# Optimization experiments

Measured on AMD Instinct MI355X. Metric: run time of the kernel, lower is better.

The kernel has to match this reference:

```python
import jax, jax.numpy as jnp
import numpy as np

N, E, D, H, O = 100000, 1600000, 128, 64, 64


def setup_inputs() -> dict:
    key = jax.random.key(0)
    ks = jax.random.split(key, 6)
    src = jax.random.randint(ks[0], (E,), 0, N)
    dst = jax.random.randint(ks[1], (E,), 0, N)
    emb = jax.random.normal(ks[2], (N, D), jnp.float32) * 0.02  # embedding table
    W1 = jax.random.normal(ks[3], (D, H), jnp.float32) / np.sqrt(D)
    b1 = jnp.zeros((H,), jnp.float32)
    W2 = jax.random.normal(ks[4], (H, O), jnp.float32) / np.sqrt(H)
    b2 = jnp.zeros((O,), jnp.float32)
    return dict(emb=emb, W1=W1, b1=b1, W2=W2, b2=b2, src=src, dst=dst)


def gcn_conv(x, W, b, src, dst):
    # PyG GCNConv: add self-loops, symmetric deg^{-1/2} norm, linear -> gather -> scatter-add, bias
    n = x.shape[0]
    loop = jnp.arange(n, dtype=src.dtype)
    s = jnp.concatenate([src, loop])
    d = jnp.concatenate([dst, loop])
    x = x @ W  # [n, out]
    deg = jax.ops.segment_sum(jnp.ones_like(d, dtype=x.dtype), d, num_segments=n)
    dinv = jnp.where(deg > 0, jax.lax.rsqrt(deg), 0.0)
    norm = dinv[s] * dinv[d]  # [E+n]
    out = jax.ops.segment_sum(x[s] * norm[:, None], d, num_segments=n)
    return out + b


def reference(emb, W1, b1, W2, b2, src, dst):
    # node_ids = unique(edge_index) == arange(N) for contiguous ids -> lookup is whole table
    x = emb
    x = jax.nn.relu(gcn_conv(x, W1, b1, src, dst))
    return gcn_conv(x, W2, b2, src, dst)
```

## Files before the change

kernel.cpp:

```cpp
#include <hip/hip_runtime.h>

constexpr int FD = 64;
constexpr int P  = 8;
constexpr int WN = 125;
constexpr int SRC_BITS = 17;
constexpr int SRC_MASK = (1 << SRC_BITS) - 1;
constexpr int G1S = 16;

__device__ __forceinline__ int part_of(int d, unsigned long long M) {
    return (int)(((unsigned long long)(unsigned)d * M) >> 32);
}

__device__ __forceinline__ unsigned bf16pack(float a, float b) {
    unsigned ua = __float_as_uint(a), ub = __float_as_uint(b);
    ua = (ua + 0x7FFFu + ((ua >> 16) & 1u)) >> 16;
    ub = (ub + 0x7FFFu + ((ub >> 16) & 1u)) >> 16;
    return ua | (ub << 16);
}
__device__ __forceinline__ float4 bf16x4(uint2 u) {
    float4 v;
    v.x = __uint_as_float(u.x << 16);
    v.y = __uint_as_float(u.x & 0xFFFF0000u);
    v.z = __uint_as_float(u.y << 16);
    v.w = __uint_as_float(u.y & 0xFFFF0000u);
    return v;
}

__global__ void k_init(int* __restrict__ gcur1, int cap1,
                       int* __restrict__ gcur2, int cap2, int NW) {
    int i = threadIdx.x;
    if (i < P)  gcur1[i * G1S] = i * cap1;
    if (i < NW) gcur2[i] = i * cap2;
}

__global__ __launch_bounds__(256) void k_part8(const int* __restrict__ src,
                                               const int* __restrict__ dst, int E,
                                               unsigned long long M, int npp,
                                               int* __restrict__ gcur1, int cap1,
                                               int* __restrict__ p1) {
    constexpr int CH = 1024;
    __shared__ int hh[P], bbase[P], lcur[P];
    if (threadIdx.x < P) hh[threadIdx.x] = 0;
    __syncthreads();
    const int e0  = blockIdx.x * CH;
    const int rem = min(CH, E - e0);
    const int lane = threadIdx.x & 63;
    const unsigned long long lmlt = (lane == 63) ? ~0ull >> 1 : (1ull << lane) - 1;

    int dv[4], sv[4], bv[4], ldr[4], rnk[4], cnt[4];
    bool val[4];
    unsigned long long mm[4];
#pragma unroll
    for (int j = 0; j < 4; ++j) {
        int i = j * 256 + threadIdx.x;
        val[j] = i < rem;
        int e = e0 + (val[j] ? i : 0);
        dv[j] = __builtin_nontemporal_load(&dst[e]);
        sv[j] = __builtin_nontemporal_load(&src[e]);
        bv[j] = part_of(dv[j], M);
    }
#pragma unroll
    for (int j = 0; j < 4; ++j) {
        unsigned long long m0 = __ballot(val[j] && (bv[j] & 1));
        unsigned long long m1 = __ballot(val[j] && (bv[j] & 2));
        unsigned long long m2 = __ballot(val[j] && (bv[j] & 4));
        unsigned long long mv = __ballot(val[j]);
        unsigned long long t = ((bv[j] & 1) ? m0 : ~m0)
                             & ((bv[j] & 2) ? m1 : ~m1)
                             & ((bv[j] & 4) ? m2 : ~m2) & mv;
        mm[j]  = t;
        ldr[j] = __ffsll((unsigned long long)t) - 1;
        rnk[j] = __popcll(t & lmlt);
        cnt[j] = __popcll(t);
        if (val[j] && lane == ldr[j]) atomicAdd(&hh[bv[j]], cnt[j]);
    }
    __syncthreads();
    if (threadIdx.x < P) {
        bbase[threadIdx.x] = atomicAdd(&gcur1[threadIdx.x * G1S], hh[threadIdx.x]);
        lcur[threadIdx.x] = 0;
    }
    __syncthreads();
#pragma unroll
    for (int j = 0; j < 4; ++j) {
        int wb = 0;
        if (val[j] && lane == ldr[j]) wb = atomicAdd(&lcur[bv[j]], cnt[j]);
        wb = __shfl(wb, ldr[j] < 0 ? 0 : ldr[j], 64);
        if (val[j]) {
            int pos = bbase[bv[j]] + wb + rnk[j];
            if (pos < (bv[j] + 1) * cap1)
                p1[pos] = ((dv[j] - bv[j] * npp) << SRC_BITS) | sv[j];
        }
    }
}

__global__ __launch_bounds__(256) void k_partwin(const int* __restrict__ p1,
                                                 const int* __restrict__ gcur1, int cap1,
                                                 int npp, unsigned long long M2,
                                                 int* __restrict__ gcur2, int cap2,
                                                 int* __restrict__ p2) {
    constexpr int CH = 1024;
    constexpr int MAXW = 128;
    __shared__ int hh[MAXW], wbase[MAXW], lcur[MAXW];
    const int p   = blockIdx.x & (P - 1);
    const int j   = blockIdx.x >> 3;
    const int wlo = (p * npp) / WN;
    const int whi = ((p + 1) * npp - 1) / WN;
    const int nw  = whi - wlo + 1;
    const int lo = p * cap1 + j * CH;
    const int hi = min(lo + CH, gcur1[p * G1S]);
    if (lo >= hi) return;
    for (int t = threadIdx.x; t < nw; t += 256) hh[t] = 0;
    __syncthreads();
    int pk[4], wv[4];
    bool val[4];
#pragma unroll
    for (int q = 0; q < 4; ++q) {
        int e = lo + q * 256 + threadIdx.x;
        val[q] = e < hi;
        pk[q] = val[q] ? __builtin_nontemporal_load(&p1[e]) : 0;
        int d = p * npp + (pk[q] >> SRC_BITS);
        wv[q] = (int)(((unsigned long long)(unsigned)d * M2) >> 32);
        if (val[q]) atomicAdd(&hh[wv[q] - wlo], 1);
    }
    __syncthreads();
    for (int t = threadIdx.x; t < nw; t += 256) {
        wbase[t] = hh[t] ? atomicAdd(&gcur2[wlo + t], hh[t]) : 0;
        lcur[t] = 0;
    }
    __syncthreads();
#pragma unroll
    for (int q = 0; q < 4; ++q) {
        if (val[q]) {
            int w  = wv[q];
            int hw = w - wlo;
            int d  = p * npp + (pk[q] >> SRC_BITS);
            int pos = wbase[hw] + atomicAdd(&lcur[hw], 1);
            if (pos < (w + 1) * cap2)
                p2[pos] = ((d - w * WN) << SRC_BITS) | (pk[q] & SRC_MASK);
        }
    }
}

__global__ __launch_bounds__(256) void k_sortwin(int* __restrict__ p2,
                                                 const int* __restrict__ gcur2, int cap2,
                                                 int* __restrict__ rowinfo,
                                                 float* __restrict__ dinv, int N) {
    __shared__ int hist[WN], beg[WN], cur[WN];
    const int w  = blockIdx.x;
    const int lo = w * cap2;
    const int hi = min(gcur2[w], lo + cap2);
    const int cnt = hi - lo;
    for (int t = threadIdx.x; t < WN; t += 256) hist[t] = 0;
    __syncthreads();
    int pk[10];
#pragma unroll
    for (int j = 0; j < 10; ++j) {
        int i = j * 256 + threadIdx.x;
        pk[j] = (i < cnt) ? p2[lo + i] : -1;
        if (pk[j] >= 0) atomicAdd(&hist[pk[j] >> SRC_BITS], 1);
    }
    __syncthreads();
    if (threadIdx.x < 64) {
        int lane = threadIdx.x;
        int v0 = hist[lane];
        int x0 = v0;
#pragma unroll
        for (int o = 1; o < 64; o <<= 1) { int y = __shfl_up(x0, o, 64); if (lane >= o) x0 += y; }
        int tot0 = __shfl(x0, 63, 64);
        int v1 = (lane < WN - 64) ? hist[64 + lane] : 0;
        int x1 = v1;
#pragma unroll
        for (int o = 1; o < 64; o <<= 1) { int y = __shfl_up(x1, o, 64); if (lane >= o) x1 += y; }
        int b0 = x0 - v0;
        beg[lane] = b0; cur[lane] = b0;
        if (lane < WN - 64) {
            int b1 = tot0 + x1 - v1;
            beg[64 + lane] = b1; cur[64 + lane] = b1;
        }
    }
    __syncthreads();
#pragma unroll
    for (int j = 0; j < 10; ++j) {
        if (pk[j] >= 0) {
            int ld  = pk[j] >> SRC_BITS;
            int pos = atomicAdd(&cur[ld], 1);
            p2[lo + pos] = pk[j] & SRC_MASK;
        }
    }
    for (int t = threadIdx.x; t < WN; t += 256) {
        int node = w * WN + t;
        if (node < N) {
            rowinfo[node] = beg[t] | (hist[t] << 16);
            dinv[node] = rsqrtf((float)(hist[t] + 1));
        }
    }
}

template <int K, bool RELU>
__global__ __launch_bounds__(256) void k_gemm(const float* __restrict__ X,
                                              const float* __restrict__ W,
                                              const float* __restrict__ dinv,
                                              unsigned* __restrict__ Yb, int n) {
    constexpr int ASTR = 260;
    __shared__ __align__(16) float Bs[K * FD];
    __shared__ __align__(16) float As[32 * ASTR];
    for (int i = threadIdx.x; i < K * FD / 4; i += 256)
        ((float4*)Bs)[i] = ((const float4*)W)[i];

    const int rt   = threadIdx.x >> 3;
    const int ct   = threadIdx.x & 7;
    const int row0 = blockIdx.x * 256;
    float acc[8][8] = {};

    for (int kp = 0; kp < K; kp += 32) {
        __syncthreads();
        const int mq = threadIdx.x >> 3;
        const int q  = threadIdx.x & 7;
        float4 tv[8];
#pragma unroll
        for (int pass = 0; pass < 8; ++pass) {
            int grow = row0 + mq + pass * 32;
            float4 v = make_float4(0.f, 0.f, 0.f, 0.f);
            if (grow < n) {
                v = *(const float4*)&X[(size_t)grow * K + kp + q * 4];
                if (RELU) {
                    v.x = fmaxf(v.x, 0.f); v.y = fmaxf(v.y, 0.f);
                    v.z = fmaxf(v.z, 0.f); v.w = fmaxf(v.w, 0.f);
                }
            }
            tv[pass] = v;
        }
#pragma unroll
        for (int pass = 0; pass < 8; ++pass) {
            int m = mq + pass * 32;
            As[(q * 4 + 0) * ASTR + m] = tv[pass].x;
            As[(q * 4 + 1) * ASTR + m] = tv[pass].y;
            As[(q * 4 + 2) * ASTR + m] = tv[pass].z;
            As[(q * 4 + 3) * ASTR + m] = tv[pass].w;
        }
        __syncthreads();
#pragma unroll 8
        for (int k = 0; k < 32; ++k) {
            float4 a0 = *(const float4*)&As[k * ASTR + rt * 8];
            float4 a1 = *(const float4*)&As[k * ASTR + rt * 8 + 4];
            float4 b0 = *(const float4*)&Bs[(kp + k) * FD + ct * 8];
            float4 b1 = *(const float4*)&Bs[(kp + k) * FD + ct * 8 + 4];
            float af[8] = {a0.x, a0.y, a0.z, a0.w, a1.x, a1.y, a1.z, a1.w};
            float bf[8] = {b0.x, b0.y, b0.z, b0.w, b1.x, b1.y, b1.z, b1.w};
#pragma unroll
            for (int i = 0; i < 8; ++i)
#pragma unroll
                for (int j = 0; j < 8; ++j)
                    acc[i][j] = fmaf(af[i], bf[j], acc[i][j]);
        }
    }
#pragma unroll
    for (int i = 0; i < 8; ++i) {
        int r = row0 + rt * 8 + i;
        if (r < n) {
            float sc = dinv[r];
            uint4 w;
            w.x = bf16pack(acc[i][0] * sc, acc[i][1] * sc);
            w.y = bf16pack(acc[i][2] * sc, acc[i][3] * sc);
            w.z = bf16pack(acc[i][4] * sc, acc[i][5] * sc);
            w.w = bf16pack(acc[i][6] * sc, acc[i][7] * sc);
            ((uint4*)Yb)[(size_t)r * 8 + ct] = w;
        }
    }
}

__global__ __launch_bounds__(256) void k_agg(const unsigned* __restrict__ Xb,
                                             const int* __restrict__ col,
                                             const int* __restrict__ rowinfo, int cap2,
                                             const float* __restrict__ dinv,
                                             const float* __restrict__ bias,
                                             float* __restrict__ out, int n) {
    int t = blockIdx.x * 256 + threadIdx.x;
    int node = t >> 4;
    int lane = t & 15;
    if (node >= n) return;
    int info = rowinfo[node];
    int w    = (int)((unsigned)node / WN);
    int beg  = w * cap2 + (info & 0xFFFF);
    int end  = beg + (info >> 16);
    const uint2* Xv = (const uint2*)Xb;
    uint2 svu = Xv[(size_t)node * 16 + lane];
    float4 a0 = {0,0,0,0}, a1 = {0,0,0,0}, a2 = {0,0,0,0}, a3 = {0,0,0,0};
    int e = beg;
    for (; e + 8 <= end; e += 8) {
        int s0 = col[e],     s1 = col[e + 1], s2 = col[e + 2], s3 = col[e + 3];
        int s4 = col[e + 4], s5 = col[e + 5], s6 = col[e + 6], s7 = col[e + 7];
        uint2 u0 = Xv[(size_t)s0 * 16 + lane];
        uint2 u1 = Xv[(size_t)s1 * 16 + lane];
        uint2 u2 = Xv[(size_t)s2 * 16 + lane];
        uint2 u3 = Xv[(size_t)s3 * 16 + lane];
        uint2 u4 = Xv[(size_t)s4 * 16 + lane];
        uint2 u5 = Xv[(size_t)s5 * 16 + lane];
        uint2 u6 = Xv[(size_t)s6 * 16 + lane];
        uint2 u7 = Xv[(size_t)s7 * 16 + lane];
        float4 v0 = bf16x4(u0), v1 = bf16x4(u1), v2 = bf16x4(u2), v3 = bf16x4(u3);
        float4 v4 = bf16x4(u4), v5 = bf16x4(u5), v6 = bf16x4(u6), v7 = bf16x4(u7);
        a0.x += v0.x; a0.y += v0.y; a0.z += v0.z; a0.w += v0.w;
        a1.x += v1.x; a1.y += v1.y; a1.z += v1.z; a1.w += v1.w;
        a2.x += v2.x; a2.y += v2.y; a2.z += v2.z; a2.w += v2.w;
        a3.x += v3.x; a3.y += v3.y; a3.z += v3.z; a3.w += v3.w;
        a0.x += v4.x; a0.y += v4.y; a0.z += v4.z; a0.w += v4.w;
        a1.x += v5.x; a1.y += v5.y; a1.z += v5.z; a1.w += v5.w;
        a2.x += v6.x; a2.y += v6.y; a2.z += v6.z; a2.w += v6.w;
        a3.x += v7.x; a3.y += v7.y; a3.z += v7.z; a3.w += v7.w;
    }
    for (; e + 4 <= end; e += 4) {
        int s0 = col[e], s1 = col[e + 1], s2 = col[e + 2], s3 = col[e + 3];
        uint2 u0 = Xv[(size_t)s0 * 16 + lane];
        uint2 u1 = Xv[(size_t)s1 * 16 + lane];
        uint2 u2 = Xv[(size_t)s2 * 16 + lane];
        uint2 u3 = Xv[(size_t)s3 * 16 + lane];
        float4 v0 = bf16x4(u0), v1 = bf16x4(u1), v2 = bf16x4(u2), v3 = bf16x4(u3);
        a0.x += v0.x; a0.y += v0.y; a0.z += v0.z; a0.w += v0.w;
        a1.x += v1.x; a1.y += v1.y; a1.z += v1.z; a1.w += v1.w;
        a2.x += v2.x; a2.y += v2.y; a2.z += v2.z; a2.w += v2.w;
        a3.x += v3.x; a3.y += v3.y; a3.z += v3.z; a3.w += v3.w;
    }
    for (; e < end; ++e) {
        float4 v = bf16x4(Xv[(size_t)col[e] * 16 + lane]);
        a0.x += v.x; a0.y += v.y; a0.z += v.z; a0.w += v.w;
    }
    float4 sv = bf16x4(svu);
    float sx = a0.x + a1.x + a2.x + a3.x + sv.x;
    float sy = a0.y + a1.y + a2.y + a3.y + sv.y;
    float sz = a0.z + a1.z + a2.z + a3.z + sv.z;
    float sw = a0.w + a1.w + a2.w + a3.w + sv.w;
    float di = dinv[node];
    float4 b = ((const float4*)bias)[lane];
    float4 o;
    o.x = fmaf(di, sx, b.x);
    o.y = fmaf(di, sy, b.y);
    o.z = fmaf(di, sz, b.z);
    o.w = fmaf(di, sw, b.w);
    ((float4*)(out + (size_t)node * FD))[lane] = o;
}


extern "C" void kernel_launch(void* const* d_in, const int* in_sizes, int n_in,
                              void* d_out, int out_size, void* d_ws, size_t ws_size,
                              hipStream_t stream) {
    const float* emb = (const float*)d_in[0];
    const float* W1  = (const float*)d_in[1];
    const float* b1  = (const float*)d_in[2];
    const float* W2  = (const float*)d_in[3];
    const float* b2  = (const float*)d_in[4];
    const int*   src = (const int*)d_in[5];
    const int*   dst = (const int*)d_in[6];

    const int D = 128;
    const int N = in_sizes[0] / D;
    const int E = in_sizes[5];
    float* out = (float*)d_out;

    const int npp  = (N + P - 1) / P;
    const int NW   = (N + WN - 1) / WN;
    const int cap1 = E / P + 16384;
    int cap2 = E / NW + 560;
    if (cap2 > 2560) cap2 = 2560;

    const unsigned long long M  = ((1ull << 32) + npp - 1) / npp;
    const unsigned long long M2 = ((1ull << 32) + WN - 1) / WN;

    unsigned* Ab   = (unsigned*)d_ws;
    int*   p2      = (int*)(Ab + (size_t)N * 32);
    int*   rowinfo = p2 + (size_t)NW * cap2;
    float* dinv    = (float*)(rowinfo + N);
    int*   gcur1   = (int*)(dinv + N);
    int*   gcur2   = gcur1 + P * G1S;
    int*   p1      = gcur2 + NW;

    k_init<<<1, 1024, 0, stream>>>(gcur1, cap1, gcur2, cap2, NW);
    k_part8<<<(E + 1023) / 1024, 256, 0, stream>>>(src, dst, E, M, npp, gcur1, cap1, p1);
    int nb2 = (cap1 + 1023) / 1024;
    k_partwin<<<P * nb2, 256, 0, stream>>>(p1, gcur1, cap1, npp, M2, gcur2, cap2, p2);
    k_sortwin<<<NW, 256, 0, stream>>>(p2, gcur2, cap2, rowinfo, dinv, N);

    int gblocks = (N + 255) / 256;
    k_gemm<128, false><<<gblocks, 256, 0, stream>>>(emb, W1, dinv, Ab, N);
    k_agg<<<(N * 16 + 255) / 256, 256, 0, stream>>>(Ab, p2, rowinfo, cap2, dinv, b1, out, N);
    k_gemm<64, true><<<gblocks, 256, 0, stream>>>(out, W2, dinv, Ab, N);
    k_agg<<<(N * 16 + 255) / 256, 256, 0, stream>>>(Ab, p2, rowinfo, cap2, dinv, b2, out, N);
}
```

Baseline: 199.8 us.

## Use bf16 MFMA for GEMMs and store hidden layer as bf16

Replaces the fp32 shared-memory FMA GEMM with a bf16 MFMA 16x16x32 kernel that reads pre-transposed bf16 weights, produced by a new small transpose kernel. The first aggregation now applies ReLU and writes the hidden activations in bf16 into the output buffer, which halves the traffic of the second GEMM's input. The partition buffer p1 is aliased onto the Ab workspace. In exchange the GEMM inputs are rounded to bf16, which lowers precision, and the output stores are scattered 2-byte writes.

```diff
diff --git a/kernel.cpp b/kernel.cpp
--- a/kernel.cpp
+++ b/kernel.cpp
@@ -7,17 +7,23 @@
 constexpr int SRC_MASK = (1 << SRC_BITS) - 1;
 constexpr int G1S = 16;
 
+typedef __attribute__((ext_vector_type(8))) short bf16x8;
+typedef __attribute__((ext_vector_type(4))) float f32x4;
+
 __device__ __forceinline__ int part_of(int d, unsigned long long M) {
     return (int)(((unsigned long long)(unsigned)d * M) >> 32);
 }
-
+__device__ __forceinline__ unsigned short bf16r(float x) {
+    unsigned u = __float_as_uint(x);
+    return (unsigned short)((u + 0x7FFFu + ((u >> 16) & 1u)) >> 16);
+}
 __device__ __forceinline__ unsigned bf16pack(float a, float b) {
     unsigned ua = __float_as_uint(a), ub = __float_as_uint(b);
     ua = (ua + 0x7FFFu + ((ua >> 16) & 1u)) >> 16;
     ub = (ub + 0x7FFFu + ((ub >> 16) & 1u)) >> 16;
     return ua | (ub << 16);
 }
-__device__ __forceinline__ float4 bf16x4(uint2 u) {
+__device__ __forceinline__ float4 bf16x4u(uint2 u) {
     float4 v;
     v.x = __uint_as_float(u.x << 16);
     v.y = __uint_as_float(u.x & 0xFFFF0000u);
@@ -49,7 +55,6 @@
 
     int dv[4], sv[4], bv[4], ldr[4], rnk[4], cnt[4];
     bool val[4];
-    unsigned long long mm[4];
 #pragma unroll
     for (int j = 0; j < 4; ++j) {
         int i = j * 256 + threadIdx.x;
@@ -68,7 +73,6 @@
         unsigned long long t = ((bv[j] & 1) ? m0 : ~m0)
                              & ((bv[j] & 2) ? m1 : ~m1)
                              & ((bv[j] & 4) ? m2 : ~m2) & mv;
-        mm[j]  = t;
         ldr[j] = __ffsll((unsigned long long)t) - 1;
         rnk[j] = __popcll(t & lmlt);
         cnt[j] = __popcll(t);
@@ -196,85 +200,82 @@
     }
 }
 
-template <int K, bool RELU>
-__global__ __launch_bounds__(256) void k_gemm(const float* __restrict__ X,
-                                              const float* __restrict__ W,
-                                              const float* __restrict__ dinv,
-                                              unsigned* __restrict__ Yb, int n) {
-    constexpr int ASTR = 260;
-    __shared__ __align__(16) float Bs[K * FD];
-    __shared__ __align__(16) float As[32 * ASTR];
-    for (int i = threadIdx.x; i < K * FD / 4; i += 256)
-        ((float4*)Bs)[i] = ((const float4*)W)[i];
-
-    const int rt   = threadIdx.x >> 3;
-    const int ct   = threadIdx.x & 7;
-    const int row0 = blockIdx.x * 256;
-    float acc[8][8] = {};
-
-    for (int kp = 0; kp < K; kp += 32) {
-        __syncthreads();
-        const int mq = threadIdx.x >> 3;
-        const int q  = threadIdx.x & 7;
-        float4 tv[8];
-#pragma unroll
-        for (int pass = 0; pass < 8; ++pass) {
-            int grow = row0 + mq + pass * 32;
-            float4 v = make_float4(0.f, 0.f, 0.f, 0.f);
-            if (grow < n) {
-                v = *(const float4*)&X[(size_t)grow * K + kp + q * 4];
-                if (RELU) {
-                    v.x = fmaxf(v.x, 0.f); v.y = fmaxf(v.y, 0.f);
-                    v.z = fmaxf(v.z, 0.f); v.w = fmaxf(v.w, 0.f);
-                }
+__global__ void k_wt(const float* __restrict__ W1, const float* __restrict__ W2,
+                     unsigned short* __restrict__ Wt1, unsigned short* __restrict__ Wt2) {
+    int i = blockIdx.x * 256 + threadIdx.x;
+    if (i < 64 * 128) {
+        int c = i >> 7, k = i & 127;
+        Wt1[i] = bf16r(W1[(size_t)k * 64 + c]);
+    }
+    int j = i - 64 * 128;
+    if (j >= 0 && j < 64 * 64) {
+        int c = j >> 6, k = j & 63;
+        Wt2[j] = bf16r(W2[(size_t)k * 64 + c]);
+    }
+}
+
+template <int K, bool ABF16>
+__global__ __launch_bounds__(256) void k_gemm_mfma(const void* __restrict__ Xv,
+                                                   const uint4* __restrict__ Wt,
+                                                   const float* __restrict__ dinv,
+                                                   unsigned short* __restrict__ Yb,
+                                                   int n) {
+    constexpr int NT  = K / 32;
+    constexpr int RQ4 = K / 8;
+    const int wv = threadIdx.x >> 6;
+    const int l  = threadIdx.x & 63;
+    const int r  = l & 15, hi = l >> 4;
+    const int row = blockIdx.x * 64 + wv * 16 + r;
+    const float* Xf = (const float*)Xv;
+    const uint4* Xb = (const uint4*)Xv;
+    union U { uint4 u; bf16x8 v; };
+    f32x4 acc[4] = {};
+
+#pragma unroll
+    for (int t = 0; t < NT; ++t) {
+        U a;
+        if (ABF16) {
+            if (row < n) a.u = Xb[(size_t)row * RQ4 + t * 4 + hi];
+            else         a.u = make_uint4(0u, 0u, 0u, 0u);
+        } else {
+            float4 f0 = make_float4(0.f, 0.f, 0.f, 0.f);
+            float4 f1 = make_float4(0.f, 0.f, 0.f, 0.f);
+            if (row < n) {
+                f0 = *(const float4*)&Xf[(size_t)row * K + t * 32 + hi * 8];
+                f1 = *(const float4*)&Xf[(size_t)row * K + t * 32 + hi * 8 + 4];
             }
-            tv[pass] = v;
-        }
-#pragma unroll
-        for (int pass = 0; pass < 8; ++pass) {
-            int m = mq + pass * 32;
-            As[(q * 4 + 0) * ASTR + m] = tv[pass].x;
-            As[(q * 4 + 1) * ASTR + m] = tv[pass].y;
-            As[(q * 4 + 2) * ASTR + m] = tv[pass].z;
-            As[(q * 4 + 3) * ASTR + m] = tv[pass].w;
-        }
-        __syncthreads();
-#pragma unroll 8
-        for (int k = 0; k < 32; ++k) {
-            float4 a0 = *(const float4*)&As[k * ASTR + rt * 8];
-            float4 a1 = *(const float4*)&As[k * ASTR + rt * 8 + 4];
-            float4 b0 = *(const float4*)&Bs[(kp + k) * FD + ct * 8];
-            float4 b1 = *(const float4*)&Bs[(kp + k) * FD + ct * 8 + 4];
-            float af[8] = {a0.x, a0.y, a0.z, a0.w, a1.x, a1.y, a1.z, a1.w};
-            float bf[8] = {b0.x, b0.y, b0.z, b0.w, b1.x, b1.y, b1.z, b1.w};
-#pragma unroll
-            for (int i = 0; i < 8; ++i)
-#pragma unroll
-                for (int j = 0; j < 8; ++j)
-                    acc[i][j] = fmaf(af[i], bf[j], acc[i][j]);
-        }
-    }
-#pragma unroll
-    for (int i = 0; i < 8; ++i) {
-        int r = row0 + rt * 8 + i;
-        if (r < n) {
-            float sc = dinv[r];
-            uint4 w;
-            w.x = bf16pack(acc[i][0] * sc, acc[i][1] * sc);
-            w.y = bf16pack(acc[i][2] * sc, acc[i][3] * sc);
-            w.z = bf16pack(acc[i][4] * sc, acc[i][5] * sc);
-            w.w = bf16pack(acc[i][6] * sc, acc[i][7] * sc);
-            ((uint4*)Yb)[(size_t)r * 8 + ct] = w;
-        }
-    }
-}
-
+            a.u.x = bf16pack(f0.x, f0.y);
+            a.u.y = bf16pack(f0.z, f0.w);
+            a.u.z = bf16pack(f1.x, f1.y);
+            a.u.w = bf16pack(f1.z, f1.w);
+        }
+#pragma unroll
+        for (int cb = 0; cb < 4; ++cb) {
+            U b;
+            b.u = Wt[(size_t)(cb * 16 + r) * RQ4 + t * 4 + hi];
+            acc[cb] = __builtin_amdgcn_mfma_f32_16x16x32_bf16(a.v, b.v, acc[cb], 0, 0, 0);
+        }
+    }
+    const int orow0 = blockIdx.x * 64 + wv * 16 + hi * 4;
+#pragma unroll
+    for (int j = 0; j < 4; ++j) {
+        int orow = orow0 + j;
+        if (orow < n) {
+            float sc = dinv[orow];
+#pragma unroll
+            for (int cb = 0; cb < 4; ++cb)
+                Yb[(size_t)orow * 64 + cb * 16 + r] = bf16r(acc[cb][j] * sc);
+        }
+    }
+}
+
+template <bool OUTB>
 __global__ __launch_bounds__(256) void k_agg(const unsigned* __restrict__ Xb,
                                              const int* __restrict__ col,
                                              const int* __restrict__ rowinfo, int cap2,
                                              const float* __restrict__ dinv,
                                              const float* __restrict__ bias,
-                                             float* __restrict__ out, int n) {
+                                             void* __restrict__ outp, int n) {
     int t = blockIdx.x * 256 + threadIdx.x;
     int node = t >> 4;
     int lane = t & 15;
@@ -298,8 +299,8 @@
         uint2 u5 = Xv[(size_t)s5 * 16 + lane];
         uint2 u6 = Xv[(size_t)s6 * 16 + lane];
         uint2 u7 = Xv[(size_t)s7 * 16 + lane];
-        float4 v0 = bf16x4(u0), v1 = bf16x4(u1), v2 = bf16x4(u2), v3 = bf16x4(u3);
-        float4 v4 = bf16x4(u4), v5 = bf16x4(u5), v6 = bf16x4(u6), v7 = bf16x4(u7);
+        float4 v0 = bf16x4u(u0), v1 = bf16x4u(u1), v2 = bf16x4u(u2), v3 = bf16x4u(u3);
+        float4 v4 = bf16x4u(u4), v5 = bf16x4u(u5), v6 = bf16x4u(u6), v7 = bf16x4u(u7);
         a0.x += v0.x; a0.y += v0.y; a0.z += v0.z; a0.w += v0.w;
         a1.x += v1.x; a1.y += v1.y; a1.z += v1.z; a1.w += v1.w;
         a2.x += v2.x; a2.y += v2.y; a2.z += v2.z; a2.w += v2.w;
@@ -315,29 +316,38 @@
         uint2 u1 = Xv[(size_t)s1 * 16 + lane];
         uint2 u2 = Xv[(size_t)s2 * 16 + lane];
         uint2 u3 = Xv[(size_t)s3 * 16 + lane];
-        float4 v0 = bf16x4(u0), v1 = bf16x4(u1), v2 = bf16x4(u2), v3 = bf16x4(u3);
+        float4 v0 = bf16x4u(u0), v1 = bf16x4u(u1), v2 = bf16x4u(u2), v3 = bf16x4u(u3);
         a0.x += v0.x; a0.y += v0.y; a0.z += v0.z; a0.w += v0.w;
         a1.x += v1.x; a1.y += v1.y; a1.z += v1.z; a1.w += v1.w;
         a2.x += v2.x; a2.y += v2.y; a2.z += v2.z; a2.w += v2.w;
         a3.x += v3.x; a3.y += v3.y; a3.z += v3.z; a3.w += v3.w;
     }
     for (; e < end; ++e) {
-        float4 v = bf16x4(Xv[(size_t)col[e] * 16 + lane]);
+        float4 v = bf16x4u(Xv[(size_t)col[e] * 16 + lane]);
         a0.x += v.x; a0.y += v.y; a0.z += v.z; a0.w += v.w;
     }
-    float4 sv = bf16x4(svu);
+    float4 sv = bf16x4u(svu);
     float sx = a0.x + a1.x + a2.x + a3.x + sv.x;
     float sy = a0.y + a1.y + a2.y + a3.y + sv.y;
     float sz = a0.z + a1.z + a2.z + a3.z + sv.z;
     float sw = a0.w + a1.w + a2.w + a3.w + sv.w;
     float di = dinv[node];
     float4 b = ((const float4*)bias)[lane];
-    float4 o;
-    o.x = fmaf(di, sx, b.x);
-    o.y = fmaf(di, sy, b.y);
-    o.z = fmaf(di, sz, b.z);
-    o.w = fmaf(di, sw, b.w);
-    ((float4*)(out + (size_t)node * FD))[lane] = o;
+    float ox = fmaf(di, sx, b.x);
+    float oy = fmaf(di, sy, b.y);
+    float oz = fmaf(di, sz, b.z);
+    float ow = fmaf(di, sw, b.w);
+    if (OUTB) {
+        ox = fmaxf(ox, 0.f); oy = fmaxf(oy, 0.f);
+        oz = fmaxf(oz, 0.f); ow = fmaxf(ow, 0.f);
+        uint2 pw;
+        pw.x = bf16pack(ox, oy);
+        pw.y = bf16pack(oz, ow);
+        ((uint2*)outp)[(size_t)node * 16 + lane] = pw;
+    } else {
+        float4 o = make_float4(ox, oy, oz, ow);
+        ((float4*)((float*)outp + (size_t)node * FD))[lane] = o;
+    }
 }
 
 
@@ -372,17 +382,21 @@
     float* dinv    = (float*)(rowinfo + N);
     int*   gcur1   = (int*)(dinv + N);
     int*   gcur2   = gcur1 + P * G1S;
-    int*   p1      = gcur2 + NW;
+    unsigned short* Wt1 = (unsigned short*)(gcur2 + ((NW + 3) & ~3));
+    unsigned short* Wt2 = Wt1 + 64 * 128;
+    int*   p1      = (int*)Ab;
+    unsigned* hb   = (unsigned*)d_out;
 
     k_init<<<1, 1024, 0, stream>>>(gcur1, cap1, gcur2, cap2, NW);
     k_part8<<<(E + 1023) / 1024, 256, 0, stream>>>(src, dst, E, M, npp, gcur1, cap1, p1);
     int nb2 = (cap1 + 1023) / 1024;
     k_partwin<<<P * nb2, 256, 0, stream>>>(p1, gcur1, cap1, npp, M2, gcur2, cap2, p2);
     k_sortwin<<<NW, 256, 0, stream>>>(p2, gcur2, cap2, rowinfo, dinv, N);
-
-    int gblocks = (N + 255) / 256;
-    k_gemm<128, false><<<gblocks, 256, 0, stream>>>(emb, W1, dinv, Ab, N);
-    k_agg<<<(N * 16 + 255) / 256, 256, 0, stream>>>(Ab, p2, rowinfo, cap2, dinv, b1, out, N);
-    k_gemm<64, true><<<gblocks, 256, 0, stream>>>(out, W2, dinv, Ab, N);
-    k_agg<<<(N * 16 + 255) / 256, 256, 0, stream>>>(Ab, p2, rowinfo, cap2, dinv, b2, out, N);
-}
+    k_wt<<<48, 256, 0, stream>>>(W1, W2, Wt1, Wt2);
+
+    int gblocks = (N + 63) / 64;
+    k_gemm_mfma<128, false><<<gblocks, 256, 0, stream>>>(emb, (const uint4*)Wt1, dinv, (unsigned short*)Ab, N);
+    k_agg<true><<<(N * 16 + 255) / 256, 256, 0, stream>>>(Ab, p2, rowinfo, cap2, dinv, b1, hb, N);
+    k_gemm_mfma<64, true><<<gblocks, 256, 0, stream>>>(hb, (const uint4*)Wt2, dinv, (unsigned short*)Ab, N);
+    k_agg<false><<<(N * 16 + 255) / 256, 256, 0, stream>>>(Ab, p2, rowinfo, cap2, dinv, b2, out, N);
+}
```

After: 179.5 us. 1.11x faster.
